# Kernel tuning notes

Hardware: AMD Instinct MI355X
Metric: run time of the kernel (lower is better)

## Reference

```python
import jax, jax.numpy as jnp
import numpy as np

B, H, S, D = 2, 16, 2048, 64


def setup_inputs() -> dict:
    key = jax.random.key(0)
    kq, kk, kv = jax.random.split(key, 3)
    Q = jax.random.normal(kq, (B, H, S, D), dtype=jnp.float32)
    K = jax.random.normal(kk, (B, H, S, D), dtype=jnp.float32)
    V = jax.random.normal(kv, (B, H, S, D), dtype=jnp.float32)
    return {
        "Q": Q,
        "K": K,
        "V": V,
        "is_causal": 1,
        "softmax_scale": jnp.float32(1.0 / np.sqrt(D)),
    }


def reference(Q, K, V, is_causal, softmax_scale):
    seq_len = Q.shape[2]
    # [B, H, S, S] materialized scores, as in the original module
    scores = jnp.einsum("bhqd,bhkd->bhqk", Q, K) * softmax_scale
    if is_causal:
        causal = jnp.tril(jnp.ones((seq_len, seq_len), dtype=bool))
        scores = jnp.where(causal, scores, -jnp.inf)
    P = jax.nn.softmax(scores.astype(jnp.float32), axis=-1)
    out = jnp.einsum("bhqk,bhkd->bhqd", P, V)
    return out
```

## Files before the change

### kernel.cpp

```cpp
#include <hip/hip_runtime.h>
#include <stdint.h>

#define S_  2048
#define D_  64
#define KP  72
#define NT  (S_/64)
#define BH  32
#define M2  16.0f

typedef __bf16 bf16x8 __attribute__((ext_vector_type(8)));
typedef float  f32x4  __attribute__((ext_vector_type(4)));

__global__ __launch_bounds__(512, 6) void fattn_kernel(
    const float* __restrict__ Q,
    const float* __restrict__ K,
    const float* __restrict__ V,
    const int* __restrict__ causal_p,
    const float* __restrict__ scale_p,
    float* __restrict__ O)
{
  __shared__ __bf16 Klds[64 * KP];
  __shared__ __bf16 Vlds[2][64 * KP];
  __shared__ __bf16 Plds[8][16 * KP];

  const int tid  = threadIdx.x;
  const int w    = tid >> 6;
  const int lane = tid & 63;
  const int quad = lane >> 4;
  const int n    = lane & 15;

  const int bid  = blockIdx.x;
  const int bh   = bid & 31;
  const int tileA = bid >> 5;
  const int tileB = NT - 1 - tileA;
  const long base = (long)bh * S_ * D_;
  const int causal  = *causal_p;
  const float scale = *scale_p;

  const int myTile = (w < 4) ? tileA : tileB;
  const int q0   = myTile * 64;
  const int wq   = w & 3;
  const int qrow = q0 + wq * 16 + n;

  const float qs = scale * 1.44269504f;
  bf16x8 qf[2];
  {
    const float* qp = Q + base + (long)qrow * D_;
#pragma unroll
    for (int kk = 0; kk < 2; kk++) {
      float4 a = *(const float4*)(qp + kk * 32 + quad * 8);
      float4 b = *(const float4*)(qp + kk * 32 + quad * 8 + 4);
      qf[kk][0] = (__bf16)(a.x * qs); qf[kk][1] = (__bf16)(a.y * qs);
      qf[kk][2] = (__bf16)(a.z * qs); qf[kk][3] = (__bf16)(a.w * qs);
      qf[kk][4] = (__bf16)(b.x * qs); qf[kk][5] = (__bf16)(b.y * qs);
      qf[kk][6] = (__bf16)(b.z * qs); qf[kk][7] = (__bf16)(b.w * qs);
    }
  }

  f32x4 oacc[4];
  float lpart[4];
#pragma unroll
  for (int t = 0; t < 4; t++) oacc[t] = (f32x4){0.f, 0.f, 0.f, 0.f};
#pragma unroll
  for (int r = 0; r < 4; r++) lpart[r] = 0.f;

  const int tmax = causal ? tileB : (NT - 1);

  const int krow = tid >> 3;
  const int kc8  = tid & 7;
  const int vk   = tid & 63;
  const int vc8  = tid >> 6;

  float4 pka, pkb, pva, pvb;

  auto issueLoads = [&](int kt) {
    const float* kp = K + base + (long)(kt + krow) * D_ + kc8 * 8;
    pka = *(const float4*)(kp);
    pkb = *(const float4*)(kp + 4);
    const float* vp = V + base + (long)(kt + vk) * D_ + vc8 * 8;
    pva = *(const float4*)(vp);
    pvb = *(const float4*)(vp + 4);
  };
  auto stageK = [&]() {
    bf16x8 kv;
    kv[0] = (__bf16)pka.x; kv[1] = (__bf16)pka.y; kv[2] = (__bf16)pka.z; kv[3] = (__bf16)pka.w;
    kv[4] = (__bf16)pkb.x; kv[5] = (__bf16)pkb.y; kv[6] = (__bf16)pkb.z; kv[7] = (__bf16)pkb.w;
    *(bf16x8*)(&Klds[krow * KP + kc8 * 8]) = kv;
  };
  auto stageV = [&](int buf) {
    float vv[8] = {pva.x, pva.y, pva.z, pva.w, pvb.x, pvb.y, pvb.z, pvb.w};
#pragma unroll
    for (int j = 0; j < 8; j++)
      Vlds[buf][(vc8 * 8 + j) * KP + vk] = (__bf16)vv[j];
  };

  issueLoads(0);
  stageK();
  stageV(0);
  __syncthreads();

  for (int ktile = 0; ktile <= tmax; ++ktile) {
    const int curV = ktile & 1;
    const bool haveNext = (ktile < tmax);
    if (haveNext) issueLoads((ktile + 1) * 64);

    const bool active = (!causal) || (ktile <= myTile);
    const bool diag = causal && (ktile == myTile);
    if (active) {
      const int kt = ktile * 64;
#pragma unroll
      for (int t = 0; t < 4; t++) {
        f32x4 c = (f32x4){0.f, 0.f, 0.f, 0.f};
#pragma unroll
        for (int kk = 0; kk < 2; kk++) {
          bf16x8 bfrag = *(const bf16x8*)(&Klds[(t * 16 + n) * KP + kk * 32 + quad * 8]);
          c = __builtin_amdgcn_mfma_f32_16x16x32_bf16(qf[kk], bfrag, c, 0, 0, 0);
        }
        const int kg = kt + t * 16 + n;
#pragma unroll
        for (int r = 0; r < 4; r++) {
          float s = c[r];
          if (diag) {
            int qg = q0 + wq * 16 + quad * 4 + r;
            if (kg > qg) s = -10000.f;
          }
          float p = __builtin_exp2f(s - M2);
          lpart[r] += p;
          Plds[w][(quad * 4 + r) * KP + t * 16 + n] = (__bf16)p;
        }
      }
    }

    __syncthreads();

    if (active) {
      bf16x8 pf[2];
      pf[0] = *(const bf16x8*)(&Plds[w][n * KP + quad * 8]);
      pf[1] = *(const bf16x8*)(&Plds[w][n * KP + 32 + quad * 8]);
#pragma unroll
      for (int t = 0; t < 4; t++) {
        f32x4 c = oacc[t];
#pragma unroll
        for (int kk = 0; kk < 2; kk++) {
          bf16x8 vfrag = *(const bf16x8*)(&Vlds[curV][(t * 16 + n) * KP + kk * 32 + quad * 8]);
          c = __builtin_amdgcn_mfma_f32_16x16x32_bf16(pf[kk], vfrag, c, 0, 0, 0);
        }
        oacc[t] = c;
      }
    }

    if (haveNext) { stageK(); stageV(curV ^ 1); }
    __syncthreads();
  }

#pragma unroll
  for (int r = 0; r < 4; r++) {
#pragma unroll
    for (int off = 1; off < 16; off <<= 1)
      lpart[r] += __shfl_xor(lpart[r], off, 64);
    lpart[r] = 1.0f / lpart[r];
  }
#pragma unroll
  for (int t = 0; t < 4; t++) {
#pragma unroll
    for (int r = 0; r < 4; r++) {
      float o = oacc[t][r] * lpart[r];
      O[base + (long)(q0 + wq * 16 + quad * 4 + r) * D_ + t * 16 + n] = o;
    }
  }
}

extern "C" void kernel_launch(void* const* d_in, const int* in_sizes, int n_in,
                              void* d_out, int out_size, void* d_ws, size_t ws_size,
                              hipStream_t stream) {
  (void)in_sizes; (void)n_in; (void)d_ws; (void)ws_size; (void)out_size;
  const float* Q = (const float*)d_in[0];
  const float* K = (const float*)d_in[1];
  const float* V = (const float*)d_in[2];
  const int*   causal_p = (const int*)d_in[3];
  const float* scale_p  = (const float*)d_in[4];
  float* O = (float*)d_out;

  fattn_kernel<<<dim3((NT / 2) * BH), 512, 0, stream>>>(Q, K, V, causal_p, scale_p, O);
}
```

Before: 150.9 us.

## Process paired query tiles sequentially with all waves splitting the key dimension

Before, each block ran its two causal query tiles concurrently on separate wave groups, so the group with the shorter tile sat idle for many iterations. Now all eight waves work on one query tile at a time: wave pairs share a 16-row strip and each takes half of every 64-key tile. Their partial outputs and row sums are combined through LDS that reuses the P buffer. This evens out per-block work and keeps every wave busy, at the cost of loading the K/V prefix twice, adding barriers and a reduction, and lowering the launch-bounds occupancy hint from 6 to 4.

```diff
diff --git a/kernel.cpp b/kernel.cpp
--- a/kernel.cpp
+++ b/kernel.cpp
@@ -11,7 +11,7 @@
 typedef __bf16 bf16x8 __attribute__((ext_vector_type(8)));
 typedef float  f32x4  __attribute__((ext_vector_type(4)));
 
-__global__ __launch_bounds__(512, 6) void fattn_kernel(
+__global__ __launch_bounds__(512, 4) void fattn_kernel(
     const float* __restrict__ Q,
     const float* __restrict__ K,
     const float* __restrict__ V,
@@ -28,6 +28,8 @@
   const int lane = tid & 63;
   const int quad = lane >> 4;
   const int n    = lane & 15;
+  const int strip = w >> 1;
+  const int h     = w & 1;
 
   const int bid  = blockIdx.x;
   const int bh   = bid & 31;
@@ -35,36 +37,7 @@
   const int tileB = NT - 1 - tileA;
   const long base = (long)bh * S_ * D_;
   const int causal  = *causal_p;
-  const float scale = *scale_p;
-
-  const int myTile = (w < 4) ? tileA : tileB;
-  const int q0   = myTile * 64;
-  const int wq   = w & 3;
-  const int qrow = q0 + wq * 16 + n;
-
-  const float qs = scale * 1.44269504f;
-  bf16x8 qf[2];
-  {
-    const float* qp = Q + base + (long)qrow * D_;
-#pragma unroll
-    for (int kk = 0; kk < 2; kk++) {
-      float4 a = *(const float4*)(qp + kk * 32 + quad * 8);
-      float4 b = *(const float4*)(qp + kk * 32 + quad * 8 + 4);
-      qf[kk][0] = (__bf16)(a.x * qs); qf[kk][1] = (__bf16)(a.y * qs);
-      qf[kk][2] = (__bf16)(a.z * qs); qf[kk][3] = (__bf16)(a.w * qs);
-      qf[kk][4] = (__bf16)(b.x * qs); qf[kk][5] = (__bf16)(b.y * qs);
-      qf[kk][6] = (__bf16)(b.z * qs); qf[kk][7] = (__bf16)(b.w * qs);
-    }
-  }
-
-  f32x4 oacc[4];
-  float lpart[4];
-#pragma unroll
-  for (int t = 0; t < 4; t++) oacc[t] = (f32x4){0.f, 0.f, 0.f, 0.f};
-#pragma unroll
-  for (int r = 0; r < 4; r++) lpart[r] = 0.f;
-
-  const int tmax = causal ? tileB : (NT - 1);
+  const float qs = (*scale_p) * 1.44269504f;
 
   const int krow = tid >> 3;
   const int kc8  = tid & 7;
@@ -94,34 +67,62 @@
       Vlds[buf][(vc8 * 8 + j) * KP + vk] = (__bf16)vv[j];
   };
 
-  issueLoads(0);
-  stageK();
-  stageV(0);
-  __syncthreads();
+  float* Osc = (float*)&Plds[0][0];
+  float* Lsc = Osc + 4 * 16 * 65;
 
-  for (int ktile = 0; ktile <= tmax; ++ktile) {
-    const int curV = ktile & 1;
-    const bool haveNext = (ktile < tmax);
-    if (haveNext) issueLoads((ktile + 1) * 64);
+#pragma unroll 1
+  for (int ph = 0; ph < 2; ph++) {
+    const int tq  = ph ? tileB : tileA;
+    const int q0  = tq * 64;
+    const int lim = causal ? tq : (NT - 1);
 
-    const bool active = (!causal) || (ktile <= myTile);
-    const bool diag = causal && (ktile == myTile);
-    if (active) {
-      const int kt = ktile * 64;
+    bf16x8 qf[2];
+    {
+      const float* qp = Q + base + (long)(q0 + strip * 16 + n) * D_;
 #pragma unroll
-      for (int t = 0; t < 4; t++) {
+      for (int kk = 0; kk < 2; kk++) {
+        float4 a = *(const float4*)(qp + kk * 32 + quad * 8);
+        float4 b = *(const float4*)(qp + kk * 32 + quad * 8 + 4);
+        qf[kk][0] = (__bf16)(a.x * qs); qf[kk][1] = (__bf16)(a.y * qs);
+        qf[kk][2] = (__bf16)(a.z * qs); qf[kk][3] = (__bf16)(a.w * qs);
+        qf[kk][4] = (__bf16)(b.x * qs); qf[kk][5] = (__bf16)(b.y * qs);
+        qf[kk][6] = (__bf16)(b.z * qs); qf[kk][7] = (__bf16)(b.w * qs);
+      }
+    }
+
+    f32x4 oacc[4];
+    float lpart[4];
+#pragma unroll
+    for (int t = 0; t < 4; t++) oacc[t] = (f32x4){0.f, 0.f, 0.f, 0.f};
+#pragma unroll
+    for (int r = 0; r < 4; r++) lpart[r] = 0.f;
+
+    issueLoads(0);
+    stageK();
+    stageV(0);
+    __syncthreads();
+
+    for (int kt2 = 0; kt2 <= lim; ++kt2) {
+      const int curV = kt2 & 1;
+      const bool haveNext = (kt2 < lim);
+      if (haveNext) issueLoads((kt2 + 1) * 64);
+      const bool diag = causal && (kt2 == tq);
+      const int kt = kt2 * 64;
+
+#pragma unroll
+      for (int t = 0; t < 2; t++) {
         f32x4 c = (f32x4){0.f, 0.f, 0.f, 0.f};
 #pragma unroll
         for (int kk = 0; kk < 2; kk++) {
-          bf16x8 bfrag = *(const bf16x8*)(&Klds[(t * 16 + n) * KP + kk * 32 + quad * 8]);
+          bf16x8 bfrag = *(const bf16x8*)(&Klds[(h * 32 + t * 16 + n) * KP + kk * 32 + quad * 8]);
           c = __builtin_amdgcn_mfma_f32_16x16x32_bf16(qf[kk], bfrag, c, 0, 0, 0);
         }
-        const int kg = kt + t * 16 + n;
+        const int kg = kt + h * 32 + t * 16 + n;
 #pragma unroll
         for (int r = 0; r < 4; r++) {
           float s = c[r];
           if (diag) {
-            int qg = q0 + wq * 16 + quad * 4 + r;
+            int qg = q0 + strip * 16 + quad * 4 + r;
             if (kg > qg) s = -10000.f;
           }
           float p = __builtin_exp2f(s - M2);
@@ -129,44 +130,54 @@
           Plds[w][(quad * 4 + r) * KP + t * 16 + n] = (__bf16)p;
         }
       }
+
+      __syncthreads();
+
+      {
+        bf16x8 pf = *(const bf16x8*)(&Plds[w][n * KP + quad * 8]);
+#pragma unroll
+        for (int td = 0; td < 4; td++) {
+          bf16x8 vfrag = *(const bf16x8*)(&Vlds[curV][(td * 16 + n) * KP + h * 32 + quad * 8]);
+          oacc[td] = __builtin_amdgcn_mfma_f32_16x16x32_bf16(pf, vfrag, oacc[td], 0, 0, 0);
+        }
+      }
+      if (haveNext) { stageK(); stageV(curV ^ 1); }
+      __syncthreads();
     }
 
-    __syncthreads();
-
-    if (active) {
-      bf16x8 pf[2];
-      pf[0] = *(const bf16x8*)(&Plds[w][n * KP + quad * 8]);
-      pf[1] = *(const bf16x8*)(&Plds[w][n * KP + 32 + quad * 8]);
 #pragma unroll
-      for (int t = 0; t < 4; t++) {
-        f32x4 c = oacc[t];
+    for (int r = 0; r < 4; r++) {
 #pragma unroll
-        for (int kk = 0; kk < 2; kk++) {
-          bf16x8 vfrag = *(const bf16x8*)(&Vlds[curV][(t * 16 + n) * KP + kk * 32 + quad * 8]);
-          c = __builtin_amdgcn_mfma_f32_16x16x32_bf16(pf[kk], vfrag, c, 0, 0, 0);
-        }
-        oacc[t] = c;
+      for (int off = 1; off < 16; off <<= 1)
+        lpart[r] += __shfl_xor(lpart[r], off, 64);
+    }
+    if (h == 1) {
+#pragma unroll
+      for (int td = 0; td < 4; td++)
+#pragma unroll
+        for (int r = 0; r < 4; r++)
+          Osc[(strip * 16 + quad * 4 + r) * 65 + td * 16 + n] = oacc[td][r];
+      if (n == 0) {
+#pragma unroll
+        for (int r = 0; r < 4; r++) Lsc[strip * 16 + quad * 4 + r] = lpart[r];
       }
     }
-
-    if (haveNext) { stageK(); stageV(curV ^ 1); }
     __syncthreads();
-  }
-
+    if (h == 0) {
+      float linv[4];
 #pragma unroll
-  for (int r = 0; r < 4; r++) {
+      for (int r = 0; r < 4; r++)
+        linv[r] = 1.0f / (lpart[r] + Lsc[strip * 16 + quad * 4 + r]);
 #pragma unroll
-    for (int off = 1; off < 16; off <<= 1)
-      lpart[r] += __shfl_xor(lpart[r], off, 64);
-    lpart[r] = 1.0f / lpart[r];
-  }
+      for (int td = 0; td < 4; td++) {
 #pragma unroll
-  for (int t = 0; t < 4; t++) {
-#pragma unroll
-    for (int r = 0; r < 4; r++) {
-      float o = oacc[t][r] * lpart[r];
-      O[base + (long)(q0 + wq * 16 + quad * 4 + r) * D_ + t * 16 + n] = o;
+        for (int r = 0; r < 4; r++) {
+          float o = (oacc[td][r] + Osc[(strip * 16 + quad * 4 + r) * 65 + td * 16 + n]) * linv[r];
+          O[base + (long)(q0 + strip * 16 + quad * 4 + r) * D_ + td * 16 + n] = o;
+        }
+      }
     }
+    __syncthreads();
   }
 }
 
```

New measurement: 145.4 us. 3.6% less time.
